# Kernel tuning notes

Measured on AMD Instinct MI355X. Metric: run time of the kernel, lower is better.

The kernel has to match this reference:

```python
import jax, jax.numpy as jnp
import numpy as np

EPS = 1e-12  # F.normalize eps


def sage_conv(x, src, dst, n_nodes, W_l, b_l, W_r):
    """PyG SAGEConv with mean aggregation and L2 normalize.
    out = lin_l(mean_{j in N(i)} x_j) + lin_r(x_i), then row-wise L2 normalize.
    """
    # mean-aggregate neighbor features: scatter-add then divide by in-degree
    msg_sum = jax.ops.segment_sum(x[src], dst, num_segments=n_nodes)  # [N, F]
    deg = jax.ops.segment_sum(jnp.ones_like(dst, dtype=x.dtype), dst,
                              num_segments=n_nodes)                   # [N]
    agg = msg_sum / jnp.maximum(deg, 1.0)[:, None]
    out = agg @ W_l + b_l + x @ W_r                                   # [N, out]
    norm = jnp.sqrt(jnp.sum(out * out, axis=-1, keepdims=True))
    return out / jnp.maximum(norm, EPS)


def setup_inputs() -> dict:
    key = jax.random.key(0)
    ks = jax.random.split(key, 8)
    N, E, D_IN, D_H, D_OUT = 100000, 320000, 256, 64, 4
    x = jax.random.normal(ks[0], (N, D_IN), dtype=jnp.float32)
    edge_index = jax.random.randint(ks[1], (2, E), 0, N, dtype=jnp.int32)
    s1 = 1.0 / np.sqrt(D_IN)
    s2 = 1.0 / np.sqrt(D_H)
    W1_l = jax.random.uniform(ks[2], (D_IN, D_H), jnp.float32, -s1, s1)
    b1_l = jnp.zeros((D_H,), jnp.float32)
    W1_r = jax.random.uniform(ks[3], (D_IN, D_H), jnp.float32, -s1, s1)
    W2_l = jax.random.uniform(ks[4], (D_H, D_OUT), jnp.float32, -s2, s2)
    b2_l = jnp.zeros((D_OUT,), jnp.float32)
    W2_r = jax.random.uniform(ks[5], (D_H, D_OUT), jnp.float32, -s2, s2)
    return {"x": x, "edge_index": edge_index,
            "W1_l": W1_l, "b1_l": b1_l, "W1_r": W1_r,
            "W2_l": W2_l, "b2_l": b2_l, "W2_r": W2_r}


def reference(x, edge_index, W1_l, b1_l, W1_r, W2_l, b2_l, W2_r):
    # eval mode: dropout is identity
    n_nodes = x.shape[0]
    src, dst = edge_index[0], edge_index[1]
    h = jax.nn.relu(sage_conv(x, src, dst, n_nodes, W1_l, b1_l, W1_r))
    out = sage_conv(h, src, dst, n_nodes, W2_l, b2_l, W2_r)
    return out
```

## Files before the change

### kernel.cpp

```cpp
#include <hip/hip_runtime.h>

#define DIN 256
#define DH  64
#define DOUT 4
#define CAP 32

typedef __attribute__((ext_vector_type(8))) short bf16x8;
typedef __attribute__((ext_vector_type(4))) float f32x4;

__device__ __forceinline__ short f2bf(float f) {
    unsigned int u = __float_as_uint(f);
    unsigned int r = (u + 0x7FFFu + ((u >> 16) & 1u)) >> 16;
    return (short)r;
}
__device__ __forceinline__ short f2bf_trunc(float f) {
    return (short)(__float_as_uint(f) >> 16);
}
__device__ __forceinline__ float bf2f(short h) {
    return __uint_as_float(((unsigned int)(unsigned short)h) << 16);
}

__global__ void fillprep_kernel(const int* __restrict__ src, const int* __restrict__ dst,
                                int* __restrict__ cnt, int* __restrict__ bucket,
                                const float* __restrict__ Wl, const float* __restrict__ Wr,
                                short* __restrict__ WTh, short* __restrict__ WTl,
                                int E, int FB)
{
    if ((int)blockIdx.x >= FB) {
        const int n = blockIdx.x - FB;
        const int k = threadIdx.x;
        const float v = (n < 64) ? Wl[k * 64 + n] : Wr[k * 64 + (n - 64)];
        const short hi = f2bf(v);
        const short lo = f2bf(v - bf2f(hi));
        WTh[n * 256 + k] = hi;
        WTl[n * 256 + k] = lo;
        return;
    }
    const int e = blockIdx.x * 256 + threadIdx.x;
    if (e >= E) return;
    const int d = dst[e];
    const int p = atomicAdd(&cnt[d], 1);
    if (p < CAP) bucket[(size_t)d * CAP + p] = src[e];
}

#define XS_LD 40
__global__ __launch_bounds__(256, 4) void gemm1_mfma(
    const float* __restrict__ x, const short* __restrict__ WTh,
    const short* __restrict__ WTl, float* __restrict__ y, int N)
{
    __shared__ short xsh[2][64 * XS_LD];
    __shared__ short xsl[2][64 * XS_LD];

    const int tid  = threadIdx.x;
    const int wave = tid >> 6;
    const int lane = tid & 63;
    const int lm   = lane & 15;
    const int quad = lane >> 4;
    const int brow = blockIdx.x * 64;

    const int xr    = tid >> 2;
    const int xk    = (tid & 3) * 8;
    const int row_g = brow + xr;
    const bool xvalid = (row_g < N);
    const float* xptr = x + (size_t)row_g * DIN + xk;
    const int xs_off = xr * XS_LD + xk;

    const int col0 = wave * 32 + lm;
    const size_t wb0 = (size_t)col0 * 256 + quad * 8;
    const size_t wb1 = (size_t)(col0 + 16) * 256 + quad * 8;

    f32x4 acc[4][2];
    #pragma unroll
    for (int mt = 0; mt < 4; ++mt)
        #pragma unroll
        for (int nt = 0; nt < 2; ++nt)
            acc[mt][nt] = (f32x4){0.f, 0.f, 0.f, 0.f};

    float4 a0, b0, a1, b1;
    a0 = b0 = a1 = b1 = make_float4(0.f, 0.f, 0.f, 0.f);
    if (xvalid) {
        a0 = ((const float4*)xptr)[0];
        b0 = ((const float4*)xptr)[1];
        a1 = ((const float4*)(xptr + 32))[0];
        b1 = ((const float4*)(xptr + 32))[1];
    }
    bf16x8 wh_cur[2], wl_cur[2];
    wh_cur[0] = *(const bf16x8*)(WTh + wb0);
    wh_cur[1] = *(const bf16x8*)(WTh + wb1);
    wl_cur[0] = *(const bf16x8*)(WTl + wb0);
    wl_cur[1] = *(const bf16x8*)(WTl + wb1);

    {
        bf16x8 ph, pl;
        float fv[8] = {a0.x, a0.y, a0.z, a0.w, b0.x, b0.y, b0.z, b0.w};
        #pragma unroll
        for (int j = 0; j < 8; ++j) {
            const short hi = f2bf_trunc(fv[j]);
            ph[j] = hi;
            pl[j] = f2bf_trunc(fv[j] - bf2f(hi));
        }
        *(bf16x8*)(&xsh[0][xs_off]) = ph;
        *(bf16x8*)(&xsl[0][xs_off]) = pl;
    }
    __syncthreads();

    #pragma unroll
    for (int k = 0; k < 8; ++k) {
        const int buf = k & 1;

        if (k < 6 && xvalid) {
            const int kc = (k + 2) * 32;
            if ((k & 1) == 0) {
                a0 = ((const float4*)(xptr + kc))[0];
                b0 = ((const float4*)(xptr + kc))[1];
            } else {
                a1 = ((const float4*)(xptr + kc))[0];
                b1 = ((const float4*)(xptr + kc))[1];
            }
        }
        bf16x8 wh_nxt[2], wl_nxt[2];
        if (k < 7) {
            const int kc = (k + 1) * 32;
            wh_nxt[0] = *(const bf16x8*)(WTh + wb0 + kc);
            wh_nxt[1] = *(const bf16x8*)(WTh + wb1 + kc);
            wl_nxt[0] = *(const bf16x8*)(WTl + wb0 + kc);
            wl_nxt[1] = *(const bf16x8*)(WTl + wb1 + kc);
        }

        #pragma unroll
        for (int mt = 0; mt < 4; ++mt) {
            const int aoff = (mt * 16 + lm) * XS_LD + quad * 8;
            const bf16x8 ah = *(const bf16x8*)(&xsh[buf][aoff]);
            const bf16x8 al = *(const bf16x8*)(&xsl[buf][aoff]);
            #pragma unroll
            for (int nt = 0; nt < 2; ++nt) {
                acc[mt][nt] = __builtin_amdgcn_mfma_f32_16x16x32_bf16(
                    ah, wh_cur[nt], acc[mt][nt], 0, 0, 0);
                acc[mt][nt] = __builtin_amdgcn_mfma_f32_16x16x32_bf16(
                    ah, wl_cur[nt], acc[mt][nt], 0, 0, 0);
                acc[mt][nt] = __builtin_amdgcn_mfma_f32_16x16x32_bf16(
                    al, wh_cur[nt], acc[mt][nt], 0, 0, 0);
            }
        }

        if (k < 7) {
            const float4 na = (k & 1) ? a0 : a1;
            const float4 nb = (k & 1) ? b0 : b1;
            bf16x8 ph, pl;
            float fv[8] = {na.x, na.y, na.z, na.w, nb.x, nb.y, nb.z, nb.w};
            #pragma unroll
            for (int j = 0; j < 8; ++j) {
                const short hi = f2bf_trunc(fv[j]);
                ph[j] = hi;
                pl[j] = f2bf_trunc(fv[j] - bf2f(hi));
            }
            *(bf16x8*)(&xsh[buf ^ 1][xs_off]) = ph;
            *(bf16x8*)(&xsl[buf ^ 1][xs_off]) = pl;
            #pragma unroll
            for (int nt = 0; nt < 2; ++nt) {
                wh_cur[nt] = wh_nxt[nt];
                wl_cur[nt] = wl_nxt[nt];
            }
            __syncthreads();
        }
    }

    #pragma unroll
    for (int mt = 0; mt < 4; ++mt) {
        #pragma unroll
        for (int r = 0; r < 4; ++r) {
            const int rg = brow + mt * 16 + quad * 4 + r;
            if (rg < N) {
                const int col = wave * 32 + lm;
                float* yp = y + (size_t)rg * 128 + col;
                yp[0]  = acc[mt][0][r];
                yp[16] = acc[mt][1][r];
            }
        }
    }
}

__global__ __launch_bounds__(256) void fused1_kernel(
    const float* __restrict__ y, const int* __restrict__ cnt, const int* __restrict__ bucket,
    const float* __restrict__ b1, const float* __restrict__ W2l, const float* __restrict__ W2r,
    float* __restrict__ z, int N)
{
    const int wave = threadIdx.x >> 6;
    const int lane = threadIdx.x & 63;
    const int i = blockIdx.x * 4 + wave;
    if (i >= N) return;

    const int deg = cnt[i];
    const int dd = (deg < CAP) ? deg : CAP;

    int myn = (lane < dd) ? bucket[(size_t)i * CAP + lane] : 0;

    float acc = 0.f;
    int j = 0;
    for (; j + 1 < dd; j += 2) {
        const int s0 = __shfl(myn, j, 64);
        const int s1 = __shfl(myn, j + 1, 64);
        const float v0 = y[(size_t)s0 * 128 + lane];
        const float v1 = y[(size_t)s1 * 128 + lane];
        acc += v0 + v1;
    }
    if (j < dd) {
        const int s0 = __shfl(myn, j, 64);
        acc += y[(size_t)s0 * 128 + lane];
    }

    const float dinv = 1.0f / fmaxf((float)deg, 1.0f);
    float v = acc * dinv + b1[lane] + y[(size_t)i * 128 + 64 + lane];

    float ss = v * v;
    #pragma unroll
    for (int m = 32; m >= 1; m >>= 1) ss += __shfl_xor(ss, m, 64);
    const float inv = 1.0f / fmaxf(sqrtf(ss), 1e-12f);
    const float hv = fmaxf(v * inv, 0.f);

    const float4 wl = *(const float4*)(W2l + lane * 4);
    const float4 wr = *(const float4*)(W2r + lane * 4);
    float p0 = hv * wl.x, p1 = hv * wl.y, p2 = hv * wl.z, p3 = hv * wl.w;
    float p4 = hv * wr.x, p5 = hv * wr.y, p6 = hv * wr.z, p7 = hv * wr.w;

    const bool b0 = (lane & 1) != 0;
    float s0_ = b0 ? p0 : p4;
    float s1_ = b0 ? p1 : p5;
    float s2_ = b0 ? p2 : p6;
    float s3_ = b0 ? p3 : p7;
    float q0 = (b0 ? p4 : p0) + __shfl_xor(s0_, 1, 64);
    float q1 = (b0 ? p5 : p1) + __shfl_xor(s1_, 1, 64);
    float q2 = (b0 ? p6 : p2) + __shfl_xor(s2_, 1, 64);
    float q3 = (b0 ? p7 : p3) + __shfl_xor(s3_, 1, 64);
    const bool b1b = (lane & 2) != 0;
    float t0 = b1b ? q0 : q2;
    float t1 = b1b ? q1 : q3;
    float r0 = (b1b ? q2 : q0) + __shfl_xor(t0, 2, 64);
    float r1 = (b1b ? q3 : q1) + __shfl_xor(t1, 2, 64);
    const bool b2 = (lane & 4) != 0;
    float u0 = b2 ? r0 : r1;
    float zv = (b2 ? r1 : r0) + __shfl_xor(u0, 4, 64);
    zv += __shfl_xor(zv, 8, 64);
    zv += __shfl_xor(zv, 16, 64);
    zv += __shfl_xor(zv, 32, 64);
    const int ch = 4 * (lane & 1) + ((lane & 2)) + ((lane >> 2) & 1);
    if (lane < 8) z[(size_t)i * 8 + ch] = zv;
}

__global__ void fused2_kernel(const float* __restrict__ z, const int* __restrict__ cnt,
                              const int* __restrict__ bucket, const float* __restrict__ b2,
                              float* __restrict__ out, int N)
{
    const int i = blockIdx.x * blockDim.x + threadIdx.x;
    if (i >= N) return;
    const int deg = cnt[i];
    const int dd = (deg < CAP) ? deg : CAP;
    float4 acc = make_float4(0.f, 0.f, 0.f, 0.f);
    for (int j = 0; j < dd; ++j) {
        const int s = bucket[(size_t)i * CAP + j];
        const float4 t = *(const float4*)(z + (size_t)s * 8);
        acc.x += t.x; acc.y += t.y; acc.z += t.z; acc.w += t.w;
    }
    const float dinv = 1.0f / fmaxf((float)deg, 1.0f);
    const float4 r  = *(const float4*)(z + (size_t)i * 8 + 4);
    const float4 bb = *(const float4*)(b2);
    float4 o;
    o.x = acc.x * dinv + bb.x + r.x;
    o.y = acc.y * dinv + bb.y + r.y;
    o.z = acc.z * dinv + bb.z + r.z;
    o.w = acc.w * dinv + bb.w + r.w;
    const float ss = o.x * o.x + o.y * o.y + o.z * o.z + o.w * o.w;
    const float inv = 1.0f / fmaxf(sqrtf(ss), 1e-12f);
    o.x *= inv; o.y *= inv; o.z *= inv; o.w *= inv;
    *(float4*)(out + (size_t)i * 4) = o;
}

extern "C" void kernel_launch(void* const* d_in, const int* in_sizes, int n_in,
                              void* d_out, int out_size, void* d_ws, size_t ws_size,
                              hipStream_t stream)
{
    const float* x    = (const float*)d_in[0];
    const int*   ei   = (const int*)d_in[1];
    const float* W1l  = (const float*)d_in[2];
    const float* b1l  = (const float*)d_in[3];
    const float* W1r  = (const float*)d_in[4];
    const float* W2l  = (const float*)d_in[5];
    const float* b2l  = (const float*)d_in[6];
    const float* W2r  = (const float*)d_in[7];
    float* out = (float*)d_out;

    const int N = in_sizes[0] / DIN;
    const int E = in_sizes[1] / 2;
    const int* src = ei;
    const int* dst = ei + E;

    char* ws = (char*)d_ws;
    size_t woff = 0;
    auto alloc = [&](size_t bytes) {
        void* p = ws + woff;
        woff += (bytes + 255) & ~(size_t)255;
        return p;
    };
    float* y      = (float*)alloc((size_t)N * 128 * 4);
    float* z      = (float*)alloc((size_t)N * 8 * 4);
    short* WTh    = (short*)alloc((size_t)128 * 256 * 2);
    short* WTl    = (short*)alloc((size_t)128 * 256 * 2);
    int*   cnt    = (int*)alloc((size_t)N * 4);
    int*   bucket = (int*)alloc((size_t)N * CAP * 4);

    hipMemsetAsync(cnt, 0, (size_t)N * 4, stream);

    const int FB = (E + 255) / 256;
    fillprep_kernel<<<FB + 128, 256, 0, stream>>>(src, dst, cnt, bucket,
                                                  W1l, W1r, WTh, WTl, E, FB);

    gemm1_mfma<<<(N + 63) / 64, 256, 0, stream>>>(x, WTh, WTl, y, N);

    fused1_kernel<<<(N + 3) / 4, 256, 0, stream>>>(y, cnt, bucket, b1l, W2l, W2r, z, N);

    fused2_kernel<<<(N + 255) / 256, 256, 0, stream>>>(z, cnt, bucket, b2l, out, N);
}
```

Before: 264.4 us.

## Fuse edge bucketing into GEMM launch and fold cnt zeroing into weight prep

Replaces the hipMemsetAsync with a kernel that zeroes the degree counters in the same launch as weight transposition/splitting. Edge bucketing moves into the GEMM launch as extra leading blocks, so the scatter's atomics overlap with the MFMA GEMM. The GEMM's x prefetch is shortened from two stages ahead to one, and the occupancy hint rises from 4 to 6 blocks per CU. This removes one launch plus a memset, at the cost of less latency hiding for x loads and of atomic traffic sharing the machine with the GEMM.

```diff
diff --git a/kernel.cpp b/kernel.cpp
--- a/kernel.cpp
+++ b/kernel.cpp
@@ -20,14 +20,12 @@
     return __uint_as_float(((unsigned int)(unsigned short)h) << 16);
 }
 
-__global__ void fillprep_kernel(const int* __restrict__ src, const int* __restrict__ dst,
-                                int* __restrict__ cnt, int* __restrict__ bucket,
-                                const float* __restrict__ Wl, const float* __restrict__ Wr,
-                                short* __restrict__ WTh, short* __restrict__ WTl,
-                                int E, int FB)
-{
-    if ((int)blockIdx.x >= FB) {
-        const int n = blockIdx.x - FB;
+__global__ void wprep_zero_kernel(const float* __restrict__ Wl, const float* __restrict__ Wr,
+                                  short* __restrict__ WTh, short* __restrict__ WTl,
+                                  int* __restrict__ cnt, int N)
+{
+    if ((int)blockIdx.x < 128) {
+        const int n = blockIdx.x;
         const int k = threadIdx.x;
         const float v = (n < 64) ? Wl[k * 64 + n] : Wr[k * 64 + (n - 64)];
         const short hi = f2bf(v);
@@ -36,27 +34,40 @@
         WTl[n * 256 + k] = lo;
         return;
     }
-    const int e = blockIdx.x * 256 + threadIdx.x;
-    if (e >= E) return;
-    const int d = dst[e];
-    const int p = atomicAdd(&cnt[d], 1);
-    if (p < CAP) bucket[(size_t)d * CAP + p] = src[e];
+    const int t4 = (blockIdx.x - 128) * 256 + threadIdx.x;
+    const int n4 = N >> 2;
+    if (t4 < n4) ((int4*)cnt)[t4] = make_int4(0, 0, 0, 0);
+    if (t4 == 0)
+        for (int r = N & ~3; r < N; ++r) cnt[r] = 0;
 }
 
 #define XS_LD 40
-__global__ __launch_bounds__(256, 4) void gemm1_mfma(
+__global__ __launch_bounds__(256, 6) void gemm_scatter_kernel(
     const float* __restrict__ x, const short* __restrict__ WTh,
-    const short* __restrict__ WTl, float* __restrict__ y, int N)
+    const short* __restrict__ WTl, float* __restrict__ y,
+    const int* __restrict__ src, const int* __restrict__ dst,
+    int* __restrict__ cnt, int* __restrict__ bucket,
+    int N, int E, int SB)
 {
     __shared__ short xsh[2][64 * XS_LD];
     __shared__ short xsl[2][64 * XS_LD];
+
+    if ((int)blockIdx.x < SB) {
+        const int e = blockIdx.x * 256 + threadIdx.x;
+        if (e < E) {
+            const int d = dst[e];
+            const int p = atomicAdd(&cnt[d], 1);
+            if (p < CAP) bucket[(size_t)d * CAP + p] = src[e];
+        }
+        return;
+    }
 
     const int tid  = threadIdx.x;
     const int wave = tid >> 6;
     const int lane = tid & 63;
     const int lm   = lane & 15;
     const int quad = lane >> 4;
-    const int brow = blockIdx.x * 64;
+    const int brow = (blockIdx.x - SB) * 64;
 
     const int xr    = tid >> 2;
     const int xk    = (tid & 3) * 8;
@@ -76,51 +87,46 @@
         for (int nt = 0; nt < 2; ++nt)
             acc[mt][nt] = (f32x4){0.f, 0.f, 0.f, 0.f};
 
-    float4 a0, b0, a1, b1;
-    a0 = b0 = a1 = b1 = make_float4(0.f, 0.f, 0.f, 0.f);
-    if (xvalid) {
-        a0 = ((const float4*)xptr)[0];
-        b0 = ((const float4*)xptr)[1];
-        a1 = ((const float4*)(xptr + 32))[0];
-        b1 = ((const float4*)(xptr + 32))[1];
+    {
+        float4 a, b;
+        if (xvalid) {
+            a = ((const float4*)xptr)[0];
+            b = ((const float4*)xptr)[1];
+        } else {
+            a = b = make_float4(0.f, 0.f, 0.f, 0.f);
+        }
+        bf16x8 ph, pl;
+        float fv[8] = {a.x, a.y, a.z, a.w, b.x, b.y, b.z, b.w};
+        #pragma unroll
+        for (int j = 0; j < 8; ++j) {
+            const short hi = f2bf_trunc(fv[j]);
+            ph[j] = hi;
+            pl[j] = f2bf_trunc(fv[j] - bf2f(hi));
+        }
+        *(bf16x8*)(&xsh[0][xs_off]) = ph;
+        *(bf16x8*)(&xsl[0][xs_off]) = pl;
     }
     bf16x8 wh_cur[2], wl_cur[2];
     wh_cur[0] = *(const bf16x8*)(WTh + wb0);
     wh_cur[1] = *(const bf16x8*)(WTh + wb1);
     wl_cur[0] = *(const bf16x8*)(WTl + wb0);
     wl_cur[1] = *(const bf16x8*)(WTl + wb1);
-
-    {
-        bf16x8 ph, pl;
-        float fv[8] = {a0.x, a0.y, a0.z, a0.w, b0.x, b0.y, b0.z, b0.w};
-        #pragma unroll
-        for (int j = 0; j < 8; ++j) {
-            const short hi = f2bf_trunc(fv[j]);
-            ph[j] = hi;
-            pl[j] = f2bf_trunc(fv[j] - bf2f(hi));
-        }
-        *(bf16x8*)(&xsh[0][xs_off]) = ph;
-        *(bf16x8*)(&xsl[0][xs_off]) = pl;
-    }
     __syncthreads();
 
     #pragma unroll
     for (int k = 0; k < 8; ++k) {
         const int buf = k & 1;
 
-        if (k < 6 && xvalid) {
-            const int kc = (k + 2) * 32;
-            if ((k & 1) == 0) {
-                a0 = ((const float4*)(xptr + kc))[0];
-                b0 = ((const float4*)(xptr + kc))[1];
-            } else {
-                a1 = ((const float4*)(xptr + kc))[0];
-                b1 = ((const float4*)(xptr + kc))[1];
-            }
-        }
+        float4 na, nb;
         bf16x8 wh_nxt[2], wl_nxt[2];
         if (k < 7) {
             const int kc = (k + 1) * 32;
+            if (xvalid) {
+                na = ((const float4*)(xptr + kc))[0];
+                nb = ((const float4*)(xptr + kc))[1];
+            } else {
+                na = nb = make_float4(0.f, 0.f, 0.f, 0.f);
+            }
             wh_nxt[0] = *(const bf16x8*)(WTh + wb0 + kc);
             wh_nxt[1] = *(const bf16x8*)(WTh + wb1 + kc);
             wl_nxt[0] = *(const bf16x8*)(WTl + wb0 + kc);
@@ -144,8 +150,6 @@
         }
 
         if (k < 7) {
-            const float4 na = (k & 1) ? a0 : a1;
-            const float4 nb = (k & 1) ? b0 : b1;
             bf16x8 ph, pl;
             float fv[8] = {na.x, na.y, na.z, na.w, nb.x, nb.y, nb.z, nb.w};
             #pragma unroll
@@ -261,7 +265,7 @@
         const float4 t = *(const float4*)(z + (size_t)s * 8);
         acc.x += t.x; acc.y += t.y; acc.z += t.z; acc.w += t.w;
     }
-    const float dinv = 1.0f / fmaxf((float)deg, 1.0f);
+    const float dinv = 1.0f / fmaxf((float)(deg), 1.0f);
     const float4 r  = *(const float4*)(z + (size_t)i * 8 + 4);
     const float4 bb = *(const float4*)(b2);
     float4 o;
@@ -308,13 +312,13 @@
     int*   cnt    = (int*)alloc((size_t)N * 4);
     int*   bucket = (int*)alloc((size_t)N * CAP * 4);
 
-    hipMemsetAsync(cnt, 0, (size_t)N * 4, stream);
-
-    const int FB = (E + 255) / 256;
-    fillprep_kernel<<<FB + 128, 256, 0, stream>>>(src, dst, cnt, bucket,
-                                                  W1l, W1r, WTh, WTl, E, FB);
-
-    gemm1_mfma<<<(N + 63) / 64, 256, 0, stream>>>(x, WTh, WTl, y, N);
+    const int ZB = ((N >> 2) + 255) / 256;
+    wprep_zero_kernel<<<128 + ZB, 256, 0, stream>>>(W1l, W1r, WTh, WTl, cnt, N);
+
+    const int SB = (E + 255) / 256;
+    const int NB = (N + 63) / 64;
+    gemm_scatter_kernel<<<SB + NB, 256, 0, stream>>>(x, WTh, WTl, y,
+                                                     src, dst, cnt, bucket, N, E, SB);
 
     fused1_kernel<<<(N + 3) / 4, 256, 0, stream>>>(y, cnt, bucket, b1l, W2l, W2r, z, N);
 
```

Measured after the change: 275.3 us. 4.1% more time.

## Process two nodes per wave in fused1 and batch neighbor loads in fused2

Applied to the files above, without the earlier changes.

The first-layer aggregation kernel now assigns two nodes to each wave and interleaves their neighbor gathers, which exposes more independent memory loads per wave and halves the grid size. The second-layer aggregation issues up to eight neighbor loads up front, unrolled, before accumulating, so the gather latency overlaps. The GEMM's x prefetch is simplified from two stages ahead to one stage ahead, which reduces register use but may expose more load latency. Padding loads for missing neighbors fetch valid but unused rows.

```diff
diff --git a/kernel.cpp b/kernel.cpp
--- a/kernel.cpp
+++ b/kernel.cpp
@@ -76,51 +76,46 @@
         for (int nt = 0; nt < 2; ++nt)
             acc[mt][nt] = (f32x4){0.f, 0.f, 0.f, 0.f};
 
-    float4 a0, b0, a1, b1;
-    a0 = b0 = a1 = b1 = make_float4(0.f, 0.f, 0.f, 0.f);
-    if (xvalid) {
-        a0 = ((const float4*)xptr)[0];
-        b0 = ((const float4*)xptr)[1];
-        a1 = ((const float4*)(xptr + 32))[0];
-        b1 = ((const float4*)(xptr + 32))[1];
+    {
+        float4 a, b;
+        if (xvalid) {
+            a = ((const float4*)xptr)[0];
+            b = ((const float4*)xptr)[1];
+        } else {
+            a = b = make_float4(0.f, 0.f, 0.f, 0.f);
+        }
+        bf16x8 ph, pl;
+        float fv[8] = {a.x, a.y, a.z, a.w, b.x, b.y, b.z, b.w};
+        #pragma unroll
+        for (int j = 0; j < 8; ++j) {
+            const short hi = f2bf_trunc(fv[j]);
+            ph[j] = hi;
+            pl[j] = f2bf_trunc(fv[j] - bf2f(hi));
+        }
+        *(bf16x8*)(&xsh[0][xs_off]) = ph;
+        *(bf16x8*)(&xsl[0][xs_off]) = pl;
     }
     bf16x8 wh_cur[2], wl_cur[2];
     wh_cur[0] = *(const bf16x8*)(WTh + wb0);
     wh_cur[1] = *(const bf16x8*)(WTh + wb1);
     wl_cur[0] = *(const bf16x8*)(WTl + wb0);
     wl_cur[1] = *(const bf16x8*)(WTl + wb1);
-
-    {
-        bf16x8 ph, pl;
-        float fv[8] = {a0.x, a0.y, a0.z, a0.w, b0.x, b0.y, b0.z, b0.w};
-        #pragma unroll
-        for (int j = 0; j < 8; ++j) {
-            const short hi = f2bf_trunc(fv[j]);
-            ph[j] = hi;
-            pl[j] = f2bf_trunc(fv[j] - bf2f(hi));
-        }
-        *(bf16x8*)(&xsh[0][xs_off]) = ph;
-        *(bf16x8*)(&xsl[0][xs_off]) = pl;
-    }
     __syncthreads();
 
     #pragma unroll
     for (int k = 0; k < 8; ++k) {
         const int buf = k & 1;
 
-        if (k < 6 && xvalid) {
-            const int kc = (k + 2) * 32;
-            if ((k & 1) == 0) {
-                a0 = ((const float4*)(xptr + kc))[0];
-                b0 = ((const float4*)(xptr + kc))[1];
-            } else {
-                a1 = ((const float4*)(xptr + kc))[0];
-                b1 = ((const float4*)(xptr + kc))[1];
-            }
-        }
+        float4 na, nb;
         bf16x8 wh_nxt[2], wl_nxt[2];
         if (k < 7) {
             const int kc = (k + 1) * 32;
+            if (xvalid) {
+                na = ((const float4*)(xptr + kc))[0];
+                nb = ((const float4*)(xptr + kc))[1];
+            } else {
+                na = nb = make_float4(0.f, 0.f, 0.f, 0.f);
+            }
             wh_nxt[0] = *(const bf16x8*)(WTh + wb0 + kc);
             wh_nxt[1] = *(const bf16x8*)(WTh + wb1 + kc);
             wl_nxt[0] = *(const bf16x8*)(WTl + wb0 + kc);
@@ -144,8 +139,6 @@
         }
 
         if (k < 7) {
-            const float4 na = (k & 1) ? a0 : a1;
-            const float4 nb = (k & 1) ? b0 : b1;
             bf16x8 ph, pl;
             float fv[8] = {na.x, na.y, na.z, na.w, nb.x, nb.y, nb.z, nb.w};
             #pragma unroll
@@ -180,49 +173,9 @@
     }
 }
 
-__global__ __launch_bounds__(256) void fused1_kernel(
-    const float* __restrict__ y, const int* __restrict__ cnt, const int* __restrict__ bucket,
-    const float* __restrict__ b1, const float* __restrict__ W2l, const float* __restrict__ W2r,
-    float* __restrict__ z, int N)
-{
-    const int wave = threadIdx.x >> 6;
-    const int lane = threadIdx.x & 63;
-    const int i = blockIdx.x * 4 + wave;
-    if (i >= N) return;
-
-    const int deg = cnt[i];
-    const int dd = (deg < CAP) ? deg : CAP;
-
-    int myn = (lane < dd) ? bucket[(size_t)i * CAP + lane] : 0;
-
-    float acc = 0.f;
-    int j = 0;
-    for (; j + 1 < dd; j += 2) {
-        const int s0 = __shfl(myn, j, 64);
-        const int s1 = __shfl(myn, j + 1, 64);
-        const float v0 = y[(size_t)s0 * 128 + lane];
-        const float v1 = y[(size_t)s1 * 128 + lane];
-        acc += v0 + v1;
-    }
-    if (j < dd) {
-        const int s0 = __shfl(myn, j, 64);
-        acc += y[(size_t)s0 * 128 + lane];
-    }
-
-    const float dinv = 1.0f / fmaxf((float)deg, 1.0f);
-    float v = acc * dinv + b1[lane] + y[(size_t)i * 128 + 64 + lane];
-
-    float ss = v * v;
-    #pragma unroll
-    for (int m = 32; m >= 1; m >>= 1) ss += __shfl_xor(ss, m, 64);
-    const float inv = 1.0f / fmaxf(sqrtf(ss), 1e-12f);
-    const float hv = fmaxf(v * inv, 0.f);
-
-    const float4 wl = *(const float4*)(W2l + lane * 4);
-    const float4 wr = *(const float4*)(W2r + lane * 4);
+__device__ __forceinline__ float gemm2_butterfly(float hv, float4 wl, float4 wr, int lane) {
     float p0 = hv * wl.x, p1 = hv * wl.y, p2 = hv * wl.z, p3 = hv * wl.w;
     float p4 = hv * wr.x, p5 = hv * wr.y, p6 = hv * wr.z, p7 = hv * wr.w;
-
     const bool b0 = (lane & 1) != 0;
     float s0_ = b0 ? p0 : p4;
     float s1_ = b0 ? p1 : p5;
@@ -243,8 +196,79 @@
     zv += __shfl_xor(zv, 8, 64);
     zv += __shfl_xor(zv, 16, 64);
     zv += __shfl_xor(zv, 32, 64);
-    const int ch = 4 * (lane & 1) + ((lane & 2)) + ((lane >> 2) & 1);
-    if (lane < 8) z[(size_t)i * 8 + ch] = zv;
+    return zv;
+}
+
+__global__ __launch_bounds__(256) void fused1_kernel(
+    const float* __restrict__ y, const int* __restrict__ cnt, const int* __restrict__ bucket,
+    const float* __restrict__ b1, const float* __restrict__ W2l, const float* __restrict__ W2r,
+    float* __restrict__ z, int N)
+{
+    const int wave = threadIdx.x >> 6;
+    const int lane = threadIdx.x & 63;
+    const int half = lane >> 5;
+    const int l5   = lane & 31;
+    const int base = (blockIdx.x * 4 + wave) * 2;
+    if (base >= N) return;
+    const int iA = base;
+    const bool hasB = (base + 1 < N);
+    const int iB = hasB ? base + 1 : base;
+
+    const int degA = cnt[iA];
+    const int degB = cnt[iB];
+    const int ddA = (degA < CAP) ? degA : CAP;
+    const int ddB = (degB < CAP) ? degB : CAP;
+
+    const int myn = bucket[(size_t)(half ? iB : iA) * CAP + l5];
+
+    float accA = 0.f, accB = 0.f;
+    const int jm = (ddA > ddB) ? ddA : ddB;
+    for (int j = 0; j < jm; j += 2) {
+        const int sA0 = __shfl(myn, j, 64);
+        const int sA1 = __shfl(myn, j + 1, 64);
+        const int sB0 = __shfl(myn, 32 + j, 64);
+        const int sB1 = __shfl(myn, 33 + j, 64);
+        const int cA0 = (j     < ddA) ? sA0 : 0;
+        const int cA1 = (j + 1 < ddA) ? sA1 : 0;
+        const int cB0 = (j     < ddB) ? sB0 : 0;
+        const int cB1 = (j + 1 < ddB) ? sB1 : 0;
+        const float vA0 = y[(size_t)cA0 * 128 + lane];
+        const float vA1 = y[(size_t)cA1 * 128 + lane];
+        const float vB0 = y[(size_t)cB0 * 128 + lane];
+        const float vB1 = y[(size_t)cB1 * 128 + lane];
+        if (j + 1 < ddA)  accA += vA0 + vA1;
+        else if (j < ddA) accA += vA0;
+        if (j + 1 < ddB)  accB += vB0 + vB1;
+        else if (j < ddB) accB += vB0;
+    }
+
+    const float dinvA = 1.0f / fmaxf((float)degA, 1.0f);
+    const float dinvB = 1.0f / fmaxf((float)degB, 1.0f);
+    const float bl = b1[lane];
+    float vA = accA * dinvA + bl + y[(size_t)iA * 128 + 64 + lane];
+    float vB = accB * dinvB + bl + y[(size_t)iB * 128 + 64 + lane];
+
+    float ssA = vA * vA, ssB = vB * vB;
+    #pragma unroll
+    for (int m = 32; m >= 1; m >>= 1) {
+        ssA += __shfl_xor(ssA, m, 64);
+        ssB += __shfl_xor(ssB, m, 64);
+    }
+    const float invA = 1.0f / fmaxf(sqrtf(ssA), 1e-12f);
+    const float invB = 1.0f / fmaxf(sqrtf(ssB), 1e-12f);
+    const float hvA = fmaxf(vA * invA, 0.f);
+    const float hvB = fmaxf(vB * invB, 0.f);
+
+    const float4 wl = *(const float4*)(W2l + lane * 4);
+    const float4 wr = *(const float4*)(W2r + lane * 4);
+    const float zvA = gemm2_butterfly(hvA, wl, wr, lane);
+    const float zvB = gemm2_butterfly(hvB, wl, wr, lane);
+
+    const int ch = 4 * (lane & 1) + (lane & 2) + ((lane >> 2) & 1);
+    if (lane < 8) {
+        z[(size_t)iA * 8 + ch] = zvA;
+        if (hasB) z[(size_t)iB * 8 + ch] = zvB;
+    }
 }
 
 __global__ void fused2_kernel(const float* __restrict__ z, const int* __restrict__ cnt,
@@ -255,12 +279,28 @@
     if (i >= N) return;
     const int deg = cnt[i];
     const int dd = (deg < CAP) ? deg : CAP;
+
+    float4 t[8];
+    #pragma unroll
+    for (int j = 0; j < 8; ++j) {
+        int s = bucket[(size_t)i * CAP + ((j < dd) ? j : 0)];
+        s = (j < dd) ? s : i;
+        t[j] = *(const float4*)(z + (size_t)s * 8);
+    }
+
     float4 acc = make_float4(0.f, 0.f, 0.f, 0.f);
-    for (int j = 0; j < dd; ++j) {
+    #pragma unroll
+    for (int j = 0; j < 8; ++j) {
+        if (j < dd) {
+            acc.x += t[j].x; acc.y += t[j].y; acc.z += t[j].z; acc.w += t[j].w;
+        }
+    }
+    for (int j = 8; j < dd; ++j) {
         const int s = bucket[(size_t)i * CAP + j];
-        const float4 t = *(const float4*)(z + (size_t)s * 8);
-        acc.x += t.x; acc.y += t.y; acc.z += t.z; acc.w += t.w;
-    }
+        const float4 u = *(const float4*)(z + (size_t)s * 8);
+        acc.x += u.x; acc.y += u.y; acc.z += u.z; acc.w += u.w;
+    }
+
     const float dinv = 1.0f / fmaxf((float)deg, 1.0f);
     const float4 r  = *(const float4*)(z + (size_t)i * 8 + 4);
     const float4 bb = *(const float4*)(b2);
@@ -316,7 +356,7 @@
 
     gemm1_mfma<<<(N + 63) / 64, 256, 0, stream>>>(x, WTh, WTl, y, N);
 
-    fused1_kernel<<<(N + 3) / 4, 256, 0, stream>>>(y, cnt, bucket, b1l, W2l, W2r, z, N);
+    fused1_kernel<<<(N + 7) / 8, 256, 0, stream>>>(y, cnt, bucket, b1l, W2l, W2r, z, N);
 
     fused2_kernel<<<(N + 255) / 256, 256, 0, stream>>>(z, cnt, bucket, b2l, out, N);
 }
```

After: 255.2 us. -3.5%, faster.
